# Kernel optimization log

Measured on AMD Instinct MI355X. Metric: run time of the kernel, lower is better.

Reference implementation:

```python
import jax, jax.numpy as jnp
import numpy as np

B, H, W, C = 8, 64, 64, 256
CB = C // 2          # bottleneck_dim = channels // 2
COMPRESSION = 2      # max-pool factor on flattened spatial axis of phi and g


def setup_inputs() -> dict:
    key = jax.random.key(0)
    k = jax.random.split(key, 5)
    he = lambda kk, fan_in, shape: jax.random.normal(kk, shape, jnp.float32) * np.sqrt(2.0 / fan_in)
    return {
        "x": jax.random.normal(k[0], (B, H, W, C), jnp.float32),
        "W_theta": he(k[1], C, (C, CB)),
        "W_phi": he(k[2], C, (C, CB)),
        "W_g": he(k[3], C, (C, CB)),
        "W_out": he(k[4], CB, (CB, C)),
    }


def _maxpool1d(t, pool):
    # MaxPool1D(pool) along axis 1 of [B, N, C] (valid padding, stride=pool)
    b, n, c = t.shape
    return t.reshape(b, n // pool, pool, c).max(axis=2)


def reference(x, W_theta, W_phi, W_g, W_out):
    b, h, w, c = x.shape
    n = h * w
    xf = x.reshape(b, n, c)                      # flatten spatial dims
    theta = xf @ W_theta                         # [B, N, Cb] (1x1 conv, no bias)
    phi = _maxpool1d(xf @ W_phi, COMPRESSION)    # [B, N/2, Cb]
    g = _maxpool1d(xf @ W_g, COMPRESSION)        # [B, N/2, Cb]
    f = jax.nn.softmax(jnp.einsum('bnd,bmd->bnm', theta, phi), axis=-1)  # [B, N, N/2]
    y = jnp.einsum('bnm,bmd->bnd', f, g)         # [B, N, Cb]
    y = (y @ W_out).reshape(b, h, w, c)          # expand conv back to C
    return x + y                                 # add_residual=True
```

## Files before the change

### kernel.cpp

```cpp
#include <hip/hip_runtime.h>
#include <math.h>

#define BB 8
#define NN 4096
#define MM 2048
#define CC 256
#define CBD 128

typedef __attribute__((ext_vector_type(8))) short s16x8;
typedef __attribute__((ext_vector_type(8))) _Float16 f16x8;
typedef __attribute__((ext_vector_type(4))) float f32x4;
typedef __attribute__((ext_vector_type(16))) float f32x16;
typedef unsigned short u16;
typedef unsigned int u32;

__device__ __forceinline__ u16 f2bf(float f) {
    union { float f; u32 u; } v; v.f = f;
    u32 r = v.u + 0x7fffu + ((v.u >> 16) & 1u);
    return (u16)(r >> 16);
}
__device__ __forceinline__ float bf2f(u16 h) {
    union { u32 u; float f; } v; v.u = ((u32)h) << 16; return v.f;
}
__device__ __forceinline__ u16 f2h(float f) {
    union { _Float16 h; u16 u; } v; v.h = (_Float16)f; return v.u;
}
__device__ __forceinline__ u32 asu(float f) {
    union { float f; u32 u; } v; v.f = f; return v.u;
}
__device__ __forceinline__ u32 pkbf(float lo, float hi) {
    return __builtin_amdgcn_perm(asu(hi), asu(lo), 0x07060302u);
}

#define MFMA(a, b, c)    __builtin_amdgcn_mfma_f32_16x16x32_bf16(a, b, c, 0, 0, 0)
#define MFMAF(a, b, c)   __builtin_amdgcn_mfma_f32_16x16x32_f16(a, b, c, 0, 0, 0)
#define MFMA32(a, b, c)  __builtin_amdgcn_mfma_f32_32x32x16_bf16(a, b, c, 0, 0, 0)
#define MFMA32F(a, b, c) __builtin_amdgcn_mfma_f32_32x32x16_f16(a, b, c, 0, 0, 0)

__device__ __forceinline__ void gload_lds16(const u16* g, u16* l) {
    __builtin_amdgcn_global_load_lds(
        (const __attribute__((address_space(1))) void*)g,
        (__attribute__((address_space(3))) void*)l, 16, 0, 0);
}

__global__ __launch_bounds__(256) void k_split_w(
    const float* __restrict__ wt, const float* __restrict__ wp,
    const float* __restrict__ wg, const float* __restrict__ wo,
    u16* wtf, u16* wpf, u16* wgf, u16* wot) {
    int e = blockIdx.x * 256 + threadIdx.x;
    int m = blockIdx.y;
    if (m < 3) {
        const float* src = m == 0 ? wt : (m == 1 ? wp : wg);
        u16* of = m == 0 ? wtf : (m == 1 ? wpf : wgf);
        int r = e >> 7, c = e & 127;
        of[c * 256 + r] = f2h(src[e]);
    } else {
        int r = e >> 8, c = e & 255;
        wot[c * 128 + r] = f2bf(wo[e]);
    }
}

__global__ __launch_bounds__(256) void k_proj(
    const float* __restrict__ x,
    const u16* __restrict__ wtf, const u16* __restrict__ wpf,
    const u16* __restrict__ wgf,
    u16* __restrict__ th, u16* __restrict__ ph, u16* __restrict__ gt) {
    __shared__ u16 S[18176];
    const int THH = 0, PHH = 8704, GL = 13056;
    u16* sxf = S;
    u16* sw  = S + 2560;
    int tid = threadIdx.x;
    int w = tid >> 6, lane = tid & 63, q = lane >> 4, li = lane & 15;
    int r0 = blockIdx.x * 64;
    int wr2 = (w >> 1) * 32, wcc = (w & 1) * 64;
    const u16* Ws[3] = {wtf, wpf, wgf};

    f32x4 aT[2][4], aP[2][4], aG[2][4];
#pragma unroll
    for (int i = 0; i < 2; i++)
#pragma unroll
        for (int j = 0; j < 4; j++) {
            aT[i][j] = (f32x4)0.f; aP[i][j] = (f32x4)0.f; aG[i][j] = (f32x4)0.f;
        }

    int xrow = tid >> 2, xseg = tid & 3;
    const float* xbase = &x[(size_t)(r0 + xrow) * 256 + xseg * 8];
    int wcol = tid >> 2, wch = tid & 3;

    float4 cx0 = ((const float4*)xbase)[0];
    float4 cx1 = ((const float4*)xbase)[1];
    s16x8 cw[6];
#pragma unroll
    for (int u = 0; u < 6; u++)
        cw[u] = *(const s16x8*)&Ws[u >> 1][(size_t)((u & 1) * 64 + wcol) * 256 + wch * 8];

    for (int kc = 0; kc < 8; kc++) {
        {
            u16 hh[8];
            hh[0] = f2h(cx0.x); hh[1] = f2h(cx0.y);
            hh[2] = f2h(cx0.z); hh[3] = f2h(cx0.w);
            hh[4] = f2h(cx1.x); hh[5] = f2h(cx1.y);
            hh[6] = f2h(cx1.z); hh[7] = f2h(cx1.w);
            *(s16x8*)&sxf[xrow * 40 + xseg * 8] = *(s16x8*)&hh[0];
#pragma unroll
            for (int u = 0; u < 6; u++)
                *(s16x8*)&sw[(u >> 1) * 5120 + ((u & 1) * 64 + wcol) * 40 + wch * 8] = cw[u];
        }
        __syncthreads();

        float4 nx0, nx1; s16x8 nw[6];
        if (kc < 7) {
            const float* xp = xbase + (kc + 1) * 32;
            nx0 = ((const float4*)xp)[0];
            nx1 = ((const float4*)xp)[1];
#pragma unroll
            for (int u = 0; u < 6; u++)
                nw[u] = *(const s16x8*)&Ws[u >> 1][(size_t)((u & 1) * 64 + wcol) * 256 +
                                                  (kc + 1) * 32 + wch * 8];
        }

        f16x8 af[2];
#pragma unroll
        for (int i = 0; i < 2; i++)
            af[i] = *(const f16x8*)&sxf[(wr2 + i * 16 + li) * 40 + q * 8];
#pragma unroll
        for (int j = 0; j < 4; j++) {
            int col = wcc + j * 16 + li;
            f16x8 bt = *(const f16x8*)&sw[0 * 5120 + col * 40 + q * 8];
            f16x8 bp = *(const f16x8*)&sw[1 * 5120 + col * 40 + q * 8];
            f16x8 bg = *(const f16x8*)&sw[2 * 5120 + col * 40 + q * 8];
#pragma unroll
            for (int i = 0; i < 2; i++) {
                aT[i][j] = MFMAF(af[i], bt, aT[i][j]);
                aP[i][j] = MFMAF(af[i], bp, aP[i][j]);
                aG[i][j] = MFMAF(af[i], bg, aG[i][j]);
            }
        }
        __syncthreads();
        if (kc < 7) {
            cx0 = nx0; cx1 = nx1;
#pragma unroll
            for (int u = 0; u < 6; u++) cw[u] = nw[u];
        }
    }

#pragma unroll
    for (int i = 0; i < 2; i++)
#pragma unroll
        for (int j = 0; j < 4; j++) {
            int col = wcc + j * 16 + li;
#pragma unroll
            for (int reg = 0; reg < 4; reg++) {
                int row = wr2 + i * 16 + q * 4 + reg;
                S[THH + row * 136 + col] = f2h(aT[i][j][reg]);
            }
#pragma unroll
            for (int pr = 0; pr < 2; pr++) {
                int ml = (wr2 >> 1) + i * 8 + q * 2 + pr;
                float vp = fmaxf(aP[i][j][pr * 2], aP[i][j][pr * 2 + 1]);
                S[PHH + ml * 136 + col] = f2h(vp);
                float vg = fmaxf(aG[i][j][pr * 2], aG[i][j][pr * 2 + 1]);
                int ml2 = (ml & ~12) | ((ml & 4) << 1) | ((ml & 8) >> 1);
                S[GL + col * 40 + ml2] = f2bf(vg);
            }
        }
    __syncthreads();

#pragma unroll
    for (int p2 = 0; p2 < 4; p2++) {
        int u2 = tid + p2 * 256;
        int row = u2 >> 4, chk = u2 & 15;
        size_t gb = (size_t)(r0 + row) * 128 + chk * 8;
        *(s16x8*)&th[gb] = *(const s16x8*)&S[THH + row * 136 + chk * 8];
    }
    {
        int row = tid >> 3, chk = tid & 7;
        size_t gb = (size_t)((r0 >> 1) + row) * 128 + chk * 16;
        *(s16x8*)&ph[gb]     = *(const s16x8*)&S[PHH + row * 136 + chk * 16];
        *(s16x8*)&ph[gb + 8] = *(const s16x8*)&S[PHH + row * 136 + chk * 16 + 8];
    }
    {
        int col = tid >> 1, half = tid & 1;
        int b = r0 >> 12;
        int base = (r0 >> 1) & 2047;
        size_t gb = (size_t)b * (128 * 2048) + (size_t)col * 2048 + base + half * 16;
        *(s16x8*)&gt[gb]     = *(const s16x8*)&S[GL + col * 40 + half * 16];
        *(s16x8*)&gt[gb + 8] = *(const s16x8*)&S[GL + col * 40 + half * 16 + 8];
    }
}

__global__ __launch_bounds__(256, 2) void k_attn(
    const u16* __restrict__ th, const u16* __restrict__ ph,
    const u16* __restrict__ gt, u16* __restrict__ ot,
    float* __restrict__ Mv, float* __restrict__ Lv) {
    __shared__ u16 smem[17408];
    u16* skh = smem;
    u16* sg  = smem + 8192;
    int tid = threadIdx.x, w = tid >> 6, lane = tid & 63;
    int q = lane & 31, b = lane >> 5;
    int bb = blockIdx.y;
    int s = blockIdx.x & 1;
    int qt = blockIdx.x >> 1;
    int n0 = qt * 128;
    int row128 = w * 32 + q;
    size_t qrow = ((size_t)bb * 4096 + n0 + row128) * 128;

    f16x8 Qf[8];
#pragma unroll
    for (int ks = 0; ks < 8; ks++)
        Qf[ks] = *(const f16x8*)&th[qrow + ks * 16 + b * 8];

    float mrow = -INFINITY, lrow = 0.f;
    f32x16 o[4];
#pragma unroll
    for (int c = 0; c < 4; c++) o[c] = (f32x16)0.f;

    int r_hi = lane >> 4, c_hi = lane & 15;
    int r_lo = lane >> 3, c_lo = lane & 7;
    int k0 = s * 1024;

    for (int kt = 0; kt < 16; kt++) {
        int m0 = k0 + kt * 64;
        if (kt) __syncthreads();
#pragma unroll
        for (int jj = 0; jj < 4; jj++) {
            int r = w * 16 + jj * 4 + r_hi;
            int gc = c_hi ^ (r & 7);
            size_t ga = (((size_t)(bb * 2048 + m0 + r)) << 7) + gc * 8;
            gload_lds16(&ph[ga], &skh[(w * 16 + jj * 4) << 7]);
            int r2 = w * 32 + jj * 8 + r_lo;
            int gc2 = c_lo ^ (r2 & 7);
            size_t ga2 = (size_t)bb * (128 * 2048) + (size_t)r2 * 2048 + m0 + gc2 * 8;
            gload_lds16(&gt[ga2], &sg[(w * 32 + jj * 8) << 6]);
        }
        __syncthreads();

        f32x16 S[2];
        S[0] = (f32x16)0.f; S[1] = (f32x16)0.f;
        __builtin_amdgcn_s_setprio(1);
#pragma unroll
        for (int ks = 0; ks < 8; ks++) {
            int off0 = (q << 7) + (((ks * 2 + b) ^ (q & 7)) << 3);
            int r1 = 32 + q;
            int off1 = (r1 << 7) + (((ks * 2 + b) ^ (r1 & 7)) << 3);
            f16x8 a0 = *(const f16x8*)&skh[off0];
            f16x8 a1 = *(const f16x8*)&skh[off1];
            S[0] = MFMA32F(a0, Qf[ks], S[0]);
            S[1] = MFMA32F(a1, Qf[ks], S[1]);
        }
        __builtin_amdgcn_s_setprio(0);

        float t0[8];
#pragma unroll
        for (int r = 0; r < 8; r++)
            t0[r] = fmaxf(fmaxf(S[0][r], S[0][r + 8]),
                          fmaxf(S[1][r], S[1][r + 8]));
        float u0 = fmaxf(t0[0], t0[1]), u1 = fmaxf(t0[2], t0[3]);
        float u2 = fmaxf(t0[4], t0[5]), u3 = fmaxf(t0[6], t0[7]);
        float vmax = fmaxf(fmaxf(u0, u1), fmaxf(u2, u3));
        vmax = fmaxf(vmax, __shfl_xor(vmax, 32, 64));

        if (!__all(vmax - mrow <= 20.f)) {
            float nm = fmaxf(mrow, vmax);
            float alph = __expf(mrow - nm);
            mrow = nm;
            lrow *= alph;
#pragma unroll
            for (int c = 0; c < 4; c++)
#pragma unroll
                for (int r = 0; r < 16; r++) o[c][r] *= alph;
        }
        float rs0 = 0.f, rs1 = 0.f, rs2 = 0.f, rs3 = 0.f;
#pragma unroll
        for (int r = 0; r < 4; r++) {
            float p00 = __expf(S[0][r] - mrow);      S[0][r] = p00;      rs0 += p00;
            float p01 = __expf(S[0][r + 4] - mrow);  S[0][r + 4] = p01;  rs1 += p01;
            float p02 = __expf(S[0][r + 8] - mrow);  S[0][r + 8] = p02;  rs2 += p02;
            float p03 = __expf(S[0][r + 12] - mrow); S[0][r + 12] = p03; rs3 += p03;
            float p10 = __expf(S[1][r] - mrow);      S[1][r] = p10;      rs0 += p10;
            float p11 = __expf(S[1][r + 4] - mrow);  S[1][r + 4] = p11;  rs1 += p11;
            float p12 = __expf(S[1][r + 8] - mrow);  S[1][r + 8] = p12;  rs2 += p12;
            float p13 = __expf(S[1][r + 12] - mrow); S[1][r + 12] = p13; rs3 += p13;
        }
        float rs = (rs0 + rs1) + (rs2 + rs3);
        rs += __shfl_xor(rs, 32, 64);
        lrow += rs;

        __builtin_amdgcn_s_setprio(1);
#pragma unroll
        for (int t = 0; t < 4; t++) {
            int half = t >> 1, base = (t & 1) * 8;
            s16x8 Pf;
            u32* pf = (u32*)&Pf;
#pragma unroll
            for (int r2 = 0; r2 < 4; r2++)
                pf[r2] = pkbf(S[half][base + 2 * r2], S[half][base + 2 * r2 + 1]);
#pragma unroll
            for (int c = 0; c < 4; c++) {
                int ch = c * 32 + q;
                int off = (ch << 6) + (((t * 2 + b) ^ (ch & 7)) << 3);
                s16x8 gv = *(const s16x8*)&sg[off];
                o[c] = MFMA32(gv, Pf, o[c]);
            }
        }
        __builtin_amdgcn_s_setprio(0);
    }
    __syncthreads();

    u16* sc = smem;
#pragma unroll
    for (int c = 0; c < 4; c++)
#pragma unroll
        for (int r2 = 0; r2 < 8; r2++) {
            int ch = c * 32 + ((r2 & 1) << 1) + 8 * (r2 >> 1) + 4 * b;
            u32 pk = (u32)f2bf(o[c][2 * r2]) | ((u32)f2bf(o[c][2 * r2 + 1]) << 16);
            *(u32*)&sc[row128 * 136 + ch] = pk;
        }
    __syncthreads();
    size_t obase = ((size_t)s * 32768 + (size_t)bb * 4096 + n0) * 128;
    int rowy = tid >> 1;
#pragma unroll
    for (int j = 0; j < 8; j++) {
        int chk = (tid & 1) * 8 + j;
        s16x8 v = *(const s16x8*)&sc[rowy * 136 + chk * 8];
        *(s16x8*)&ot[obase + (size_t)rowy * 128 + chk * 8] = v;
    }
    if (b == 0) {
        int gi = s * 32768 + bb * 4096 + n0 + row128;
        Mv[gi] = mrow;
        Lv[gi] = lrow;
    }
}

__global__ __launch_bounds__(256) void k_out(
    const u16* __restrict__ ot, const float* __restrict__ Mv,
    const float* __restrict__ Lv, const u16* __restrict__ wot,
    const float* __restrict__ x, float* __restrict__ out) {
    __shared__ char lds_o[65536];
    u16 (*sy)[128] = (u16(*)[128])lds_o;
    u16 (*sw)[128] = (u16(*)[128])(lds_o + 32768);
    int tid = threadIdx.x, w = tid >> 6, lane = tid & 63, q = lane >> 4, li = lane & 15;
    int r0 = blockIdx.x * 128, c0 = blockIdx.y * 128;
    int wr = (w >> 1) * 64, wc = (w & 1) * 64;
    const size_t OS = (size_t)32768 * 128;

    int sr = tid >> 4;
    int cc = (tid & 15) * 8;
    int swc = tid & 15;

    float a1v[8], a2v[8];
#pragma unroll
    for (int i = 0; i < 8; i++) {
        int gr = r0 + sr + i * 16;
        float m1 = Mv[gr], m2 = Mv[32768 + gr];
        float l1 = Lv[gr], l2 = Lv[32768 + gr];
        float Mx = fmaxf(m1, m2);
        float e1 = __expf(m1 - Mx), e2 = __expf(m2 - Mx);
        float inv = 1.f / (l1 * e1 + l2 * e2);
        a1v[i] = e1 * inv;
        a2v[i] = e2 * inv;
    }

#pragma unroll
    for (int i = 0; i < 8; i++) {
        int r = sr + i * 16;
        size_t ga = (size_t)(r0 + r) * 128 + cc;
        s16x8 o1 = *(const s16x8*)&ot[ga];
        s16x8 o2 = *(const s16x8*)&ot[OS + ga];
        u32 yv[4];
#pragma unroll
        for (int e = 0; e < 4; e++) {
            float v0 = bf2f((u16)o1[2 * e])     * a1v[i] + bf2f((u16)o2[2 * e])     * a2v[i];
            float v1 = bf2f((u16)o1[2 * e + 1]) * a1v[i] + bf2f((u16)o2[2 * e + 1]) * a2v[i];
            yv[e] = pkbf(v0, v1);
        }
        int sc2 = (swc ^ (r & 7)) * 8;
        *(s16x8*)&sy[r][sc2] = *(const s16x8*)&yv[0];
        *(s16x8*)&sw[r][sc2] = *(const s16x8*)&wot[(size_t)(c0 + r) * 128 + cc];
    }
    __syncthreads();

    f32x4 acc[4][4];
#pragma unroll
    for (int i = 0; i < 4; i++)
#pragma unroll
        for (int j = 0; j < 4; j++) acc[i][j] = (f32x4)0.f;

#pragma unroll
    for (int ks = 0; ks < 4; ks++) {
        s16x8 av[4], bv[4];
#pragma unroll
        for (int i = 0; i < 4; i++) {
            int ar = wr + i * 16 + li;
            av[i] = *(const s16x8*)&sy[ar][((ks * 4 + q) ^ (ar & 7)) * 8];
            int br = wc + i * 16 + li;
            bv[i] = *(const s16x8*)&sw[br][((ks * 4 + q) ^ (br & 7)) * 8];
        }
#pragma unroll
        for (int i = 0; i < 4; i++)
#pragma unroll
            for (int j = 0; j < 4; j++)
                acc[i][j] = MFMA(av[i], bv[j], acc[i][j]);
    }

    float* sT = (float*)lds_o;
#pragma unroll
    for (int h = 0; h < 2; h++) {
        __syncthreads();
        if ((w >> 1) == h) {
#pragma unroll
            for (int i = 0; i < 4; i++)
#pragma unroll
                for (int j = 0; j < 4; j++)
#pragma unroll
                    for (int reg = 0; reg < 4; reg++)
                        sT[(i * 16 + q * 4 + reg) * 132 + wc + j * 16 + li] =
                            acc[i][j][reg];
        }
        __syncthreads();
#pragma unroll
        for (int p = 0; p < 8; p++) {
            int r = (tid >> 5) + p * 8;
            int c4 = (tid & 31) * 4;
            f32x4 yv = *(f32x4*)&sT[r * 132 + c4];
            size_t row = (size_t)(r0 + h * 64 + r);
            float4 xv = *(const float4*)&x[row * 256 + c0 + c4];
            float4 ov;
            ov.x = xv.x + yv[0]; ov.y = xv.y + yv[1];
            ov.z = xv.z + yv[2]; ov.w = xv.w + yv[3];
            *(float4*)&out[row * 256 + c0 + c4] = ov;
        }
    }
}

extern "C" void kernel_launch(void* const* d_in, const int* in_sizes, int n_in,
                              void* d_out, int out_size, void* d_ws, size_t ws_size,
                              hipStream_t stream) {
    const float* x  = (const float*)d_in[0];
    const float* wt = (const float*)d_in[1];
    const float* wp = (const float*)d_in[2];
    const float* wg = (const float*)d_in[3];
    const float* wo = (const float*)d_in[4];
    float* out = (float*)d_out;

    char* p = (char*)d_ws;
    auto alloc = [&](size_t bytes) {
        char* r = p;
        p += (bytes + 255) & ~(size_t)255;
        return r;
    };
    const size_t NT = (size_t)BB * NN * CBD;
    const size_t NP = (size_t)BB * MM * CBD;

    u16* wtf = (u16*)alloc(CC * CBD * 2);
    u16* wpf = (u16*)alloc(CC * CBD * 2);
    u16* wgf = (u16*)alloc(CC * CBD * 2);
    u16* wot = (u16*)alloc(CC * CBD * 2);
    u16* th  = (u16*)alloc(NT * 2);
    u16* ph  = (u16*)alloc(NP * 2);
    u16* gt  = (u16*)alloc(NP * 2);
    float* Mv = (float*)alloc(2 * 32768 * 4);
    float* Lv = (float*)alloc(2 * 32768 * 4);
    u16* ot  = (u16*)alloc(2 * NT * 2);

    k_split_w<<<dim3(128, 4), 256, 0, stream>>>(wt, wp, wg, wo,
                                                wtf, wpf, wgf, wot);
    k_proj<<<dim3(512), 256, 0, stream>>>(x, wtf, wpf, wgf, th, ph, gt);
    k_attn<<<dim3(64, 8), 256, 0, stream>>>(th, ph, gt, ot, Mv, Lv);
    k_out<<<dim3(256, 2), 256, 0, stream>>>(ot, Mv, Lv, wot, x, out);
}
```

Baseline: 159.0 us.

## Fuse output projection into attention kernel and drop key-split partial combine

The attention kernel now walks the full key range per query tile instead of splitting keys in two. It normalizes the accumulator by the softmax sum and applies the W_out projection plus the residual add in its epilogue, which removes the separate k_out kernel and the partial-output and max/sum buffers. Global-to-LDS async loads are replaced by register-staged prefetch of the next tile. The grid drops from 512 to 256 blocks on a 256-CU part, and the occupancy hint is removed, so parallelism and latency hiding may suffer. The epilogue also writes output with scalar, poorly coalesced stores.

```diff
diff --git a/kernel.cpp b/kernel.cpp
--- a/kernel.cpp
+++ b/kernel.cpp
@@ -36,12 +36,6 @@
 #define MFMAF(a, b, c)   __builtin_amdgcn_mfma_f32_16x16x32_f16(a, b, c, 0, 0, 0)
 #define MFMA32(a, b, c)  __builtin_amdgcn_mfma_f32_32x32x16_bf16(a, b, c, 0, 0, 0)
 #define MFMA32F(a, b, c) __builtin_amdgcn_mfma_f32_32x32x16_f16(a, b, c, 0, 0, 0)
-
-__device__ __forceinline__ void gload_lds16(const u16* g, u16* l) {
-    __builtin_amdgcn_global_load_lds(
-        (const __attribute__((address_space(1))) void*)g,
-        (__attribute__((address_space(3))) void*)l, 16, 0, 0);
-}
 
 __global__ __launch_bounds__(256) void k_split_w(
     const float* __restrict__ wt, const float* __restrict__ wp,
@@ -189,18 +183,18 @@
     }
 }
 
-__global__ __launch_bounds__(256, 2) void k_attn(
+__global__ __launch_bounds__(256) void k_attn(
     const u16* __restrict__ th, const u16* __restrict__ ph,
-    const u16* __restrict__ gt, u16* __restrict__ ot,
-    float* __restrict__ Mv, float* __restrict__ Lv) {
-    __shared__ u16 smem[17408];
+    const u16* __restrict__ gt, const u16* __restrict__ wot,
+    const float* __restrict__ x, float* __restrict__ out) {
+    __shared__ u16 smem[32768];
     u16* skh = smem;
     u16* sg  = smem + 8192;
     int tid = threadIdx.x, w = tid >> 6, lane = tid & 63;
     int q = lane & 31, b = lane >> 5;
-    int bb = blockIdx.y;
-    int s = blockIdx.x & 1;
-    int qt = blockIdx.x >> 1;
+    int bid = blockIdx.x;
+    int bb = bid & 7;
+    int qt = bid >> 3;
     int n0 = qt * 128;
     int row128 = w * 32 + q;
     size_t qrow = ((size_t)bb * 4096 + n0 + row128) * 128;
@@ -215,25 +209,34 @@
 #pragma unroll
     for (int c = 0; c < 4; c++) o[c] = (f32x16)0.f;
 
-    int r_hi = lane >> 4, c_hi = lane & 15;
-    int r_lo = lane >> 3, c_lo = lane & 7;
-    int k0 = s * 1024;
-
-    for (int kt = 0; kt < 16; kt++) {
-        int m0 = k0 + kt * 64;
-        if (kt) __syncthreads();
-#pragma unroll
-        for (int jj = 0; jj < 4; jj++) {
-            int r = w * 16 + jj * 4 + r_hi;
-            int gc = c_hi ^ (r & 7);
-            size_t ga = (((size_t)(bb * 2048 + m0 + r)) << 7) + gc * 8;
-            gload_lds16(&ph[ga], &skh[(w * 16 + jj * 4) << 7]);
-            int r2 = w * 32 + jj * 8 + r_lo;
-            int gc2 = c_lo ^ (r2 & 7);
-            size_t ga2 = (size_t)bb * (128 * 2048) + (size_t)r2 * 2048 + m0 + gc2 * 8;
-            gload_lds16(&gt[ga2], &sg[(w * 32 + jj * 8) << 6]);
-        }
-        __syncthreads();
+    int prow = tid >> 2, pchk = (tid & 3) * 4;
+    int grow = tid >> 1, gchk = (tid & 1) * 4;
+    const size_t gtb = (size_t)bb * (128 * 2048) + (size_t)grow * 2048;
+
+    s16x8 cph[4], cg[4];
+#pragma unroll
+    for (int c = 0; c < 4; c++) {
+        cph[c] = *(const s16x8*)&ph[(((size_t)(bb * 2048 + prow)) << 7) + (pchk + c) * 8];
+        cg[c]  = *(const s16x8*)&gt[gtb + (gchk + c) * 8];
+    }
+
+    for (int kt = 0; kt < 32; kt++) {
+#pragma unroll
+        for (int c = 0; c < 4; c++) {
+            *(s16x8*)&skh[(prow << 7) + (((pchk + c) ^ (prow & 7)) << 3)] = cph[c];
+            *(s16x8*)&sg[(grow << 6) + (((gchk + c) ^ (grow & 7)) << 3)] = cg[c];
+        }
+        __syncthreads();
+
+        s16x8 nph[4], ng[4];
+        if (kt + 1 < 32) {
+            int m1 = (kt + 1) * 64;
+#pragma unroll
+            for (int c = 0; c < 4; c++) {
+                nph[c] = *(const s16x8*)&ph[(((size_t)(bb * 2048 + m1 + prow)) << 7) + (pchk + c) * 8];
+                ng[c]  = *(const s16x8*)&gt[gtb + m1 + (gchk + c) * 8];
+            }
+        }
 
         f32x16 S[2];
         S[0] = (f32x16)0.f; S[1] = (f32x16)0.f;
@@ -304,132 +307,74 @@
             }
         }
         __builtin_amdgcn_s_setprio(0);
-    }
-    __syncthreads();
-
-    u16* sc = smem;
+
+        __syncthreads();
+        if (kt + 1 < 32) {
+#pragma unroll
+            for (int c = 0; c < 4; c++) { cph[c] = nph[c]; cg[c] = ng[c]; }
+        }
+    }
+
+    u16* sy = smem;
+    u16* sw = smem + 16384;
+    float inv = 1.f / lrow;
 #pragma unroll
     for (int c = 0; c < 4; c++)
 #pragma unroll
         for (int r2 = 0; r2 < 8; r2++) {
             int ch = c * 32 + ((r2 & 1) << 1) + 8 * (r2 >> 1) + 4 * b;
-            u32 pk = (u32)f2bf(o[c][2 * r2]) | ((u32)f2bf(o[c][2 * r2 + 1]) << 16);
-            *(u32*)&sc[row128 * 136 + ch] = pk;
-        }
-    __syncthreads();
-    size_t obase = ((size_t)s * 32768 + (size_t)bb * 4096 + n0) * 128;
-    int rowy = tid >> 1;
-#pragma unroll
-    for (int j = 0; j < 8; j++) {
-        int chk = (tid & 1) * 8 + j;
-        s16x8 v = *(const s16x8*)&sc[rowy * 136 + chk * 8];
-        *(s16x8*)&ot[obase + (size_t)rowy * 128 + chk * 8] = v;
-    }
-    if (b == 0) {
-        int gi = s * 32768 + bb * 4096 + n0 + row128;
-        Mv[gi] = mrow;
-        Lv[gi] = lrow;
-    }
-}
-
-__global__ __launch_bounds__(256) void k_out(
-    const u16* __restrict__ ot, const float* __restrict__ Mv,
-    const float* __restrict__ Lv, const u16* __restrict__ wot,
-    const float* __restrict__ x, float* __restrict__ out) {
-    __shared__ char lds_o[65536];
-    u16 (*sy)[128] = (u16(*)[128])lds_o;
-    u16 (*sw)[128] = (u16(*)[128])(lds_o + 32768);
-    int tid = threadIdx.x, w = tid >> 6, lane = tid & 63, q = lane >> 4, li = lane & 15;
-    int r0 = blockIdx.x * 128, c0 = blockIdx.y * 128;
-    int wr = (w >> 1) * 64, wc = (w & 1) * 64;
-    const size_t OS = (size_t)32768 * 128;
-
-    int sr = tid >> 4;
-    int cc = (tid & 15) * 8;
-    int swc = tid & 15;
-
-    float a1v[8], a2v[8];
-#pragma unroll
-    for (int i = 0; i < 8; i++) {
-        int gr = r0 + sr + i * 16;
-        float m1 = Mv[gr], m2 = Mv[32768 + gr];
-        float l1 = Lv[gr], l2 = Lv[32768 + gr];
-        float Mx = fmaxf(m1, m2);
-        float e1 = __expf(m1 - Mx), e2 = __expf(m2 - Mx);
-        float inv = 1.f / (l1 * e1 + l2 * e2);
-        a1v[i] = e1 * inv;
-        a2v[i] = e2 * inv;
-    }
-
-#pragma unroll
-    for (int i = 0; i < 8; i++) {
-        int r = sr + i * 16;
-        size_t ga = (size_t)(r0 + r) * 128 + cc;
-        s16x8 o1 = *(const s16x8*)&ot[ga];
-        s16x8 o2 = *(const s16x8*)&ot[OS + ga];
-        u32 yv[4];
-#pragma unroll
-        for (int e = 0; e < 4; e++) {
-            float v0 = bf2f((u16)o1[2 * e])     * a1v[i] + bf2f((u16)o2[2 * e])     * a2v[i];
-            float v1 = bf2f((u16)o1[2 * e + 1]) * a1v[i] + bf2f((u16)o2[2 * e + 1]) * a2v[i];
-            yv[e] = pkbf(v0, v1);
-        }
-        int sc2 = (swc ^ (r & 7)) * 8;
-        *(s16x8*)&sy[r][sc2] = *(const s16x8*)&yv[0];
-        *(s16x8*)&sw[r][sc2] = *(const s16x8*)&wot[(size_t)(c0 + r) * 128 + cc];
-    }
-    __syncthreads();
-
-    f32x4 acc[4][4];
-#pragma unroll
-    for (int i = 0; i < 4; i++)
-#pragma unroll
-        for (int j = 0; j < 4; j++) acc[i][j] = (f32x4)0.f;
-
-#pragma unroll
-    for (int ks = 0; ks < 4; ks++) {
-        s16x8 av[4], bv[4];
-#pragma unroll
-        for (int i = 0; i < 4; i++) {
-            int ar = wr + i * 16 + li;
-            av[i] = *(const s16x8*)&sy[ar][((ks * 4 + q) ^ (ar & 7)) * 8];
-            int br = wc + i * 16 + li;
-            bv[i] = *(const s16x8*)&sw[br][((ks * 4 + q) ^ (br & 7)) * 8];
-        }
+            u32 pk = pkbf(o[c][2 * r2] * inv, o[c][2 * r2 + 1] * inv);
+            int chunk = (ch >> 3) ^ (row128 & 7);
+            *(u32*)&sy[(row128 << 7) + (chunk << 3) + (ch & 7)] = pk;
+        }
+
+    int wr = (w >> 1) * 64, wc = (w & 1) * 64, li = lane & 15, qq = lane >> 4;
+    int wrow = tid >> 1;
+#pragma unroll
+    for (int half = 0; half < 2; half++) {
+        int c0 = half * 128;
+        __syncthreads();
+#pragma unroll
+        for (int c = 0; c < 8; c++) {
+            int chunk = (tid & 1) * 8 + c;
+            *(s16x8*)&sw[(wrow << 7) + ((chunk ^ (wrow & 7)) << 3)] =
+                *(const s16x8*)&wot[(size_t)(c0 + wrow) * 128 + chunk * 8];
+        }
+        __syncthreads();
+
+        f32x4 acc[4][4];
 #pragma unroll
         for (int i = 0; i < 4; i++)
 #pragma unroll
+            for (int j = 0; j < 4; j++) acc[i][j] = (f32x4)0.f;
+
+#pragma unroll
+        for (int ks = 0; ks < 4; ks++) {
+            s16x8 av[4], bv[4];
+#pragma unroll
+            for (int i = 0; i < 4; i++) {
+                int ar = wr + i * 16 + li;
+                av[i] = *(const s16x8*)&sy[(ar << 7) + ((((ks * 4 + qq)) ^ (ar & 7)) << 3)];
+                int br = wc + i * 16 + li;
+                bv[i] = *(const s16x8*)&sw[(br << 7) + ((((ks * 4 + qq)) ^ (br & 7)) << 3)];
+            }
+#pragma unroll
+            for (int i = 0; i < 4; i++)
+#pragma unroll
+                for (int j = 0; j < 4; j++)
+                    acc[i][j] = MFMA(av[i], bv[j], acc[i][j]);
+        }
+
+#pragma unroll
+        for (int i = 0; i < 4; i++)
+#pragma unroll
             for (int j = 0; j < 4; j++)
-                acc[i][j] = MFMA(av[i], bv[j], acc[i][j]);
-    }
-
-    float* sT = (float*)lds_o;
-#pragma unroll
-    for (int h = 0; h < 2; h++) {
-        __syncthreads();
-        if ((w >> 1) == h) {
-#pragma unroll
-            for (int i = 0; i < 4; i++)
-#pragma unroll
-                for (int j = 0; j < 4; j++)
-#pragma unroll
-                    for (int reg = 0; reg < 4; reg++)
-                        sT[(i * 16 + q * 4 + reg) * 132 + wc + j * 16 + li] =
-                            acc[i][j][reg];
-        }
-        __syncthreads();
-#pragma unroll
-        for (int p = 0; p < 8; p++) {
-            int r = (tid >> 5) + p * 8;
-            int c4 = (tid & 31) * 4;
-            f32x4 yv = *(f32x4*)&sT[r * 132 + c4];
-            size_t row = (size_t)(r0 + h * 64 + r);
-            float4 xv = *(const float4*)&x[row * 256 + c0 + c4];
-            float4 ov;
-            ov.x = xv.x + yv[0]; ov.y = xv.y + yv[1];
-            ov.z = xv.z + yv[2]; ov.w = xv.w + yv[3];
-            *(float4*)&out[row * 256 + c0 + c4] = ov;
-        }
+#pragma unroll
+                for (int reg = 0; reg < 4; reg++) {
+                    size_t grow_ = (size_t)bb * 4096 + n0 + wr + i * 16 + qq * 4 + reg;
+                    int gcol = c0 + wc + j * 16 + li;
+                    out[grow_ * 256 + gcol] = x[grow_ * 256 + gcol] + acc[i][j][reg];
+                }
     }
 }
 
@@ -459,13 +404,9 @@
     u16* th  = (u16*)alloc(NT * 2);
     u16* ph  = (u16*)alloc(NP * 2);
     u16* gt  = (u16*)alloc(NP * 2);
-    float* Mv = (float*)alloc(2 * 32768 * 4);
-    float* Lv = (float*)alloc(2 * 32768 * 4);
-    u16* ot  = (u16*)alloc(2 * NT * 2);
 
     k_split_w<<<dim3(128, 4), 256, 0, stream>>>(wt, wp, wg, wo,
                                                 wtf, wpf, wgf, wot);
     k_proj<<<dim3(512), 256, 0, stream>>>(x, wtf, wpf, wgf, th, ph, gt);
-    k_attn<<<dim3(64, 8), 256, 0, stream>>>(th, ph, gt, ot, Mv, Lv);
-    k_out<<<dim3(256, 2), 256, 0, stream>>>(ot, Mv, Lv, wot, x, out);
-}
+    k_attn<<<dim3(256), 256, 0, stream>>>(th, ph, gt, wot, x, out);
+}
```

Result: slower. 172.0 us (+8.1%).
